# Kernel tuning notes

Hardware: AMD Instinct MI355X
Metric: run time of the kernel (lower is better)

The kernel has to match this reference:

```python
import jax, jax.numpy as jnp
import numpy as np

LORA_SCALING = 1.0 / 4.0  # lora_alpha / lora_rank
NUM_HEADS = 16
HEAD_DIM = 64
ROPE_BASE = 20000.0


def rotate_half(x):
    x1, x2 = jnp.split(x, 2, axis=-1)
    return jnp.concatenate([-x2, x1], axis=-1)


def setup_inputs() -> dict:
    key = jax.random.key(0)
    ks = jax.random.split(key, 8)
    B, S, D = 8, 1024, 1024
    hidden_states = jax.random.normal(ks[0], (B, S, D), jnp.float32)
    attention_mask = jnp.zeros((B, 1, 1, S), jnp.float32)
    # real rotary tables (HF style: duplicated half-dim freqs)
    inv_freq = 1.0 / (ROPE_BASE ** (jnp.arange(0, HEAD_DIM, 2, dtype=jnp.float32) / HEAD_DIM))
    t = jnp.arange(S, dtype=jnp.float32)
    freqs = jnp.outer(t, inv_freq)                      # [S, hd/2]
    emb = jnp.concatenate([freqs, freqs], axis=-1)      # [S, hd]
    cos = jnp.broadcast_to(jnp.cos(emb)[None], (B, S, HEAD_DIM))
    sin = jnp.broadcast_to(jnp.sin(emb)[None], (B, S, HEAD_DIM))
    adapter_mask = jax.random.randint(ks[1], (B,), 0, 5, jnp.int32)
    Wqkv_weight = jax.random.normal(ks[2], (3 * D, D), jnp.float32) * 0.02
    Wqkv_bias = jax.random.normal(ks[3], (3 * D,), jnp.float32) * 0.02
    lora_A = jax.random.normal(ks[4], (5, 4, D), jnp.float32) * 0.02
    lora_B = jax.random.normal(ks[5], (5, 3 * D, 4), jnp.float32) * 0.02
    return dict(hidden_states=hidden_states, attention_mask=attention_mask,
                cos=cos, sin=sin, adapter_mask=adapter_mask,
                Wqkv_weight=Wqkv_weight, Wqkv_bias=Wqkv_bias,
                lora_A=lora_A, lora_B=lora_B)


def reference(hidden_states, attention_mask, cos, sin, adapter_mask,
              Wqkv_weight, Wqkv_bias, lora_A, lora_B):
    B, S, D = hidden_states.shape
    H, hd = NUM_HEADS, HEAD_DIM
    # fused QKV projection with per-task LoRA (gather adapters per batch row)
    base = jnp.einsum('bsd,od->bso', hidden_states, Wqkv_weight) + Wqkv_bias
    A_t = lora_A[adapter_mask]                    # [B, r, D]
    B_t = lora_B[adapter_mask]                    # [B, 3D, r]
    lo = jnp.einsum('bsd,brd->bsr', hidden_states, A_t)
    delta = jnp.einsum('bsr,bor->bso', lo, B_t) * LORA_SCALING
    qkv = (base + delta).reshape(B, S, 3, H, hd)
    q = qkv[:, :, 0].transpose(0, 2, 1, 3)        # [B,H,S,hd]
    k = qkv[:, :, 1].transpose(0, 2, 1, 3)
    v = qkv[:, :, 2].transpose(0, 2, 1, 3)
    # inline RoPE
    c = cos[:, None, :, :]
    s = sin[:, None, :, :]
    q = q * c + rotate_half(q) * s
    k = k * c + rotate_half(k) * s
    # eager SDPA
    scaling = hd ** -0.5
    scores = jnp.einsum('bhqd,bhkd->bhqk', q, k) * scaling + attention_mask
    attn = jax.nn.softmax(scores, axis=-1)
    out = jnp.einsum('bhqk,bhkd->bhqd', attn, v)
    return out.transpose(0, 2, 1, 3).reshape(B, S, H * hd)
```

## Files before the change

### kernel.cpp

```cpp
#include <hip/hip_runtime.h>
#include <hip/hip_bf16.h>
#include <stdint.h>

typedef __attribute__((ext_vector_type(8))) short short8;
typedef __attribute__((ext_vector_type(4))) float f32x4;
typedef unsigned short ushort_t;

#define MFMA16(a, b, c) __builtin_amdgcn_mfma_f32_16x16x32_bf16((a), (b), (c), 0, 0, 0)
#define EXP2F(x) __builtin_amdgcn_exp2f(x)


__device__ __forceinline__ float bf2f(unsigned short u) {
    union { unsigned int i; float f; } x; x.i = ((unsigned int)u) << 16; return x.f;
}
__device__ __forceinline__ unsigned short f2bf(float f) {
    union { float f; unsigned int i; } x; x.f = f;
    unsigned int i = x.i;
    i = i + 0x7FFFu + ((i >> 16) & 1u);
    return (unsigned short)(i >> 16);
}
__device__ __forceinline__ unsigned int pack2(float a, float b) {
    return (unsigned int)f2bf(a) | ((unsigned int)f2bf(b) << 16);
}
__device__ __forceinline__ void glds16(const void* gsrc, void* ldst) {
    __builtin_amdgcn_global_load_lds(
        (const __attribute__((address_space(1))) unsigned int*)gsrc,
        (__attribute__((address_space(3))) unsigned int*)ldst, 16, 0, 0);
}

__global__ __launch_bounds__(64) void prep_kernel(
    const float* __restrict__ hidden,
    const float* __restrict__ W,
    const float* __restrict__ loraA,
    const int* __restrict__ adapter_mask,
    ushort_t* __restrict__ Hb,
    ushort_t* __restrict__ Wb,
    float4* __restrict__ lo)
{
    int blk = blockIdx.x;
    int lane = threadIdx.x;
    if (blk < 8192) {
        int b = blk >> 10;
        int a = adapter_mask[b];
        const float* hp = hidden + (size_t)blk * 1024 + lane * 16;
        float hv[16];
        for (int j = 0; j < 16; ++j) hv[j] = hp[j];
        uint4 p0, p1;
        p0.x = pack2(hv[0], hv[1]);  p0.y = pack2(hv[2], hv[3]);
        p0.z = pack2(hv[4], hv[5]);  p0.w = pack2(hv[6], hv[7]);
        p1.x = pack2(hv[8], hv[9]);  p1.y = pack2(hv[10], hv[11]);
        p1.z = pack2(hv[12], hv[13]); p1.w = pack2(hv[14], hv[15]);
        uint4* hd = (uint4*)(Hb + (size_t)blk * 1024 + lane * 16);
        hd[0] = p0; hd[1] = p1;
        const float* Ap = loraA + (size_t)a * 4096 + lane * 16;
        float acc[4];
        for (int r = 0; r < 4; ++r) {
            const float* ap = Ap + r * 1024;
            float s = 0.f;
            for (int j = 0; j < 16; ++j) s += hv[j] * ap[j];
            acc[r] = s;
        }
        for (int off = 32; off > 0; off >>= 1)
            for (int r = 0; r < 4; ++r) acc[r] += __shfl_xor(acc[r], off);
        if (lane == 0) lo[blk] = make_float4(acc[0], acc[1], acc[2], acc[3]);
    } else {
        int row = blk - 8192;
        const float* wp = W + (size_t)row * 1024 + lane * 16;
        float wv[16];
        for (int j = 0; j < 16; ++j) wv[j] = wp[j];
        uint4 p0, p1;
        p0.x = pack2(wv[0], wv[1]);  p0.y = pack2(wv[2], wv[3]);
        p0.z = pack2(wv[4], wv[5]);  p0.w = pack2(wv[6], wv[7]);
        p1.x = pack2(wv[8], wv[9]);  p1.y = pack2(wv[10], wv[11]);
        p1.z = pack2(wv[12], wv[13]); p1.w = pack2(wv[14], wv[15]);
        uint4* wd = (uint4*)(Wb + (size_t)row * 1024 + lane * 16);
        wd[0] = p0; wd[1] = p1;
    }
}

__global__ __launch_bounds__(256) void qkv_gemm_kernel(
    const ushort_t* __restrict__ Hb,
    const ushort_t* __restrict__ Wb,
    const float* __restrict__ bias,
    const float4* __restrict__ lo,
    const float* __restrict__ loraB,
    const int* __restrict__ adapter_mask,
    const float* __restrict__ cosp,
    const float* __restrict__ sinp,
    ushort_t* __restrict__ qw,
    ushort_t* __restrict__ kw,
    ushort_t* __restrict__ vt)
{
    __shared__ __align__(16) ushort_t As[128 * 32];
    __shared__ __align__(16) ushort_t Bs[128 * 32];
    int tid = threadIdx.x;
    int wave = tid >> 6, lane = tid & 63, quad = lane >> 4, l16 = lane & 15;
    int n0 = blockIdx.x * 128;
    int m0 = blockIdx.y * 128;
    int mq = (wave >> 1) * 64, nq = (wave & 1) * 64;

    f32x4 acc[4][4];
    for (int i = 0; i < 4; ++i) for (int j = 0; j < 4; ++j) acc[i][j] = (f32x4)0.f;

    const ushort_t* gA0 = Hb + (size_t)(m0 + (tid >> 2)) * 1024 + (tid & 3) * 8;
    const ushort_t* gA1 = gA0 + (size_t)64 * 1024;
    const ushort_t* gB0 = Wb + (size_t)(n0 + (tid >> 2)) * 1024 + (tid & 3) * 8;
    const ushort_t* gB1 = gB0 + (size_t)64 * 1024;
    char* ldsA0 = (char*)As + wave * 1024;
    char* ldsA1 = ldsA0 + 4096;
    char* ldsB0 = (char*)Bs + wave * 1024;
    char* ldsB1 = ldsB0 + 4096;

    for (int kk = 0; kk < 1024; kk += 32) {
        glds16(gA0 + kk, ldsA0);
        glds16(gA1 + kk, ldsA1);
        glds16(gB0 + kk, ldsB0);
        glds16(gB1 + kk, ldsB1);
        __syncthreads();
        short8 af[4], bf[4];
        for (int mi = 0; mi < 4; ++mi)
            af[mi] = *(const short8*)&As[(mq + mi * 16 + l16) * 32 + quad * 8];
        for (int ni = 0; ni < 4; ++ni)
            bf[ni] = *(const short8*)&Bs[(nq + ni * 16 + l16) * 32 + quad * 8];
        for (int mi = 0; mi < 4; ++mi)
            for (int ni = 0; ni < 4; ++ni)
                acc[mi][ni] = MFMA16(af[mi], bf[ni], acc[mi][ni]);
        __syncthreads();
    }

    int t = n0 >> 10;
    int b = m0 >> 10;
    int a = adapter_mask[b];
    float bi[4], bb[4][4];
    int cpos[4], chh[4];
    for (int ni = 0; ni < 4; ++ni) {
        int c = n0 + nq + ni * 16 + l16;
        bi[ni] = bias[c];
        const float* Bp = loraB + ((size_t)a * 3072 + c) * 4;
        bb[ni][0] = Bp[0]; bb[ni][1] = Bp[1]; bb[ni][2] = Bp[2]; bb[ni][3] = Bp[3];
        cpos[ni] = c & 63; chh[ni] = (c >> 6) & 15;
    }
    for (int mi = 0; mi < 4; ++mi) {
        float vals[4][4];
        for (int r = 0; r < 4; ++r) {
            int m = m0 + mq + mi * 16 + quad * 4 + r;
            float4 lov = lo[m];
            for (int ni = 0; ni < 4; ++ni)
                vals[r][ni] = acc[mi][ni][r] + bi[ni]
                      + 0.25f * (lov.x * bb[ni][0] + lov.y * bb[ni][1]
                               + lov.z * bb[ni][2] + lov.w * bb[ni][3]);
        }
        int s0 = (m0 + mq + mi * 16 + quad * 4) & 1023;
        if (t < 2) {
            for (int r = 0; r < 4; ++r) {
                int s = s0 + r;
                size_t cb = ((size_t)b * 1024 + s) * 64;
                float cA = cosp[cb + l16],      sA = sinp[cb + l16];
                float cB = cosp[cb + 16 + l16], sB = sinp[cb + 16 + l16];
                float w0 = vals[r][0] * cA - vals[r][2] * sA;
                float w2 = vals[r][2] * cA + vals[r][0] * sA;
                float w1 = vals[r][1] * cB - vals[r][3] * sB;
                float w3 = vals[r][3] * cB + vals[r][1] * sB;
                float v[4] = {w0, w1, w2, w3};
                for (int ni = 0; ni < 4; ++ni) {
                    size_t bh = (size_t)b * 16 + chh[ni];
                    ushort_t ob = f2bf(v[ni]);
                    if (t == 0) qw[(bh * 1024 + s) * 64 + cpos[ni]] = ob;
                    else        kw[(bh * 1024 + s) * 64 + cpos[ni]] = ob;
                }
            }
        } else {
            for (int ni = 0; ni < 4; ++ni) {
                uint2 pk;
                pk.x = pack2(vals[0][ni], vals[1][ni]);
                pk.y = pack2(vals[2][ni], vals[3][ni]);
                size_t bh = (size_t)b * 16 + chh[ni];
                *(uint2*)&vt[(bh * 64 + cpos[ni]) * 1024 + s0] = pk;
            }
        }
    }
}

__global__ __launch_bounds__(256) void attn_kernel(
    const ushort_t* __restrict__ qw,
    const ushort_t* __restrict__ kw,
    const ushort_t* __restrict__ vt,
    const float* __restrict__ mask,
    float* __restrict__ out)
{
    __shared__ __align__(16) ushort_t Kt[2][4096];
    __shared__ __align__(16) ushort_t Vt[2][4096];
    __shared__ __align__(16) ushort_t Ps[4][32][72];
    __shared__ float mlds[1024];
    const float KSCALE = 0.125f * 1.44269504f;
    int tid = threadIdx.x;
    int wave = tid >> 6, lane = tid & 63, quad = lane >> 4, l16 = lane & 15;
    int id = blockIdx.x;
    int qt = id >> 7;
    int bh = id & 127;
    int b = bh >> 4, h = bh & 15;
    size_t base = (size_t)bh * 65536;
    int q0 = qt * 128 + wave * 32;

    for (int i = tid; i < 1024; i += 256) mlds[i] = mask[b * 1024 + i] * 1.44269504f;

    const ushort_t* kbase = kw + base;
    const ushort_t* vbase = vt + base;

    int n0 = tid, n1 = tid + 256;
    int r0 = n0 >> 3, c0 = (n0 & 7) ^ (r0 & 7);
    int r1 = n1 >> 3, c1 = (n1 & 7) ^ (r1 & 7);
    char* kd0[2] = { (char*)&Kt[0][0] + wave * 1024, (char*)&Kt[1][0] + wave * 1024 };
    char* vd0[2] = { (char*)&Vt[0][0] + wave * 1024, (char*)&Vt[1][0] + wave * 1024 };

    short8 qf[2][2];
    for (int mt = 0; mt < 2; ++mt)
        for (int kt = 0; kt < 2; ++kt)
            qf[mt][kt] = *(const short8*)(qw + base + (size_t)(q0 + mt * 16 + l16) * 64 + kt * 32 + quad * 8);

    f32x4 oacc[2][4], sum_acc[2];
    for (int mt = 0; mt < 2; ++mt) {
        sum_acc[mt] = (f32x4)0.f;
        for (int nt = 0; nt < 4; ++nt) oacc[mt][nt] = (f32x4)0.f;
    }

    short8 ones;
    for (int j = 0; j < 8; ++j) ones[j] = (short)0x3F80;

    glds16(kbase + (size_t)r0 * 64 + c0 * 8, kd0[0]);
    glds16(kbase + (size_t)r1 * 64 + c1 * 8, kd0[0] + 4096);
    glds16(vbase + (size_t)r0 * 1024 + c0 * 8, vd0[0]);
    glds16(vbase + (size_t)r1 * 1024 + c1 * 8, vd0[0] + 4096);

    int koff[4][2], voff[4][2];
    for (int nt = 0; nt < 4; ++nt)
        for (int kt = 0; kt < 2; ++kt) {
            int rr = nt * 16 + l16;
            int cc = (kt * 4 + quad) ^ (rr & 7);
            koff[nt][kt] = (rr * 8 + cc) * 8;
            voff[nt][kt] = (rr * 8 + cc) * 8;
        }

    for (int it = 0; it < 16; ++it) {
        int cur = it & 1;
        int kt0 = it * 64;
        __syncthreads();
        if (it < 15) {
            int kn = kt0 + 64;
            int nxt = cur ^ 1;
            glds16(kbase + (size_t)(kn + r0) * 64 + c0 * 8, kd0[nxt]);
            glds16(kbase + (size_t)(kn + r1) * 64 + c1 * 8, kd0[nxt] + 4096);
            glds16(vbase + (size_t)r0 * 1024 + kn + c0 * 8, vd0[nxt]);
            glds16(vbase + (size_t)r1 * 1024 + kn + c1 * 8, vd0[nxt] + 4096);
        }
        short8 kf[4][2];
        for (int nt = 0; nt < 4; ++nt)
            for (int kt = 0; kt < 2; ++kt)
                kf[nt][kt] = *(const short8*)&Kt[cur][koff[nt][kt]];
        f32x4 sacc[2][4];
        for (int mt = 0; mt < 2; ++mt)
            for (int nt = 0; nt < 4; ++nt) {
                f32x4 z = (f32x4)0.f;
                z = MFMA16(qf[mt][0], kf[nt][0], z);
                z = MFMA16(qf[mt][1], kf[nt][1], z);
                sacc[mt][nt] = z;
            }
        float mv[4];
        for (int nt = 0; nt < 4; ++nt) mv[nt] = mlds[kt0 + nt * 16 + l16];
        for (int mt = 0; mt < 2; ++mt)
            for (int nt = 0; nt < 4; ++nt)
                for (int r = 0; r < 4; ++r) {
                    float p = EXP2F(sacc[mt][nt][r] * KSCALE + mv[nt]);
                    Ps[wave][mt * 16 + quad * 4 + r][nt * 16 + l16] = f2bf(p);
                }
        short8 pf[2][2];
        for (int mt = 0; mt < 2; ++mt)
            for (int kt = 0; kt < 2; ++kt)
                pf[mt][kt] = *(const short8*)&Ps[wave][mt * 16 + l16][kt * 32 + quad * 8];
        short8 vf[4][2];
        for (int nt = 0; nt < 4; ++nt)
            for (int kt = 0; kt < 2; ++kt)
                vf[nt][kt] = *(const short8*)&Vt[cur][voff[nt][kt]];
        for (int mt = 0; mt < 2; ++mt) {
            for (int nt = 0; nt < 4; ++nt) {
                oacc[mt][nt] = MFMA16(pf[mt][0], vf[nt][0], oacc[mt][nt]);
                oacc[mt][nt] = MFMA16(pf[mt][1], vf[nt][1], oacc[mt][nt]);
            }
            sum_acc[mt] = MFMA16(pf[mt][0], ones, sum_acc[mt]);
            sum_acc[mt] = MFMA16(pf[mt][1], ones, sum_acc[mt]);
        }
    }

    for (int mt = 0; mt < 2; ++mt) {
        for (int r = 0; r < 4; ++r) {
            float inv = 1.f / sum_acc[mt][r];
            int s = q0 + mt * 16 + quad * 4 + r;
            size_t ob = ((size_t)b * 1024 + s) * 1024 + h * 64;
            for (int nt = 0; nt < 4; ++nt)
                out[ob + nt * 16 + l16] = oacc[mt][nt][r] * inv;
        }
    }
}

extern "C" void kernel_launch(void* const* d_in, const int* in_sizes, int n_in,
                              void* d_out, int out_size, void* d_ws, size_t ws_size,
                              hipStream_t stream)
{
    const float* hidden = (const float*)d_in[0];
    const float* mask   = (const float*)d_in[1];
    const float* cosp   = (const float*)d_in[2];
    const float* sinp   = (const float*)d_in[3];
    const int* adapter_mask = (const int*)d_in[4];
    const float* W      = (const float*)d_in[5];
    const float* bias   = (const float*)d_in[6];
    const float* loraA  = (const float*)d_in[7];
    const float* loraB  = (const float*)d_in[8];
    float* out = (float*)d_out;

    char* ws = (char*)d_ws;
    float4* lo = (float4*)ws;
    ushort_t* qw = (ushort_t*)(ws + (1 << 20));
    ushort_t* kw = qw + (size_t)8 * 16 * 1024 * 64;
    ushort_t* vt = kw + (size_t)8 * 16 * 1024 * 64;

    ushort_t* Hb = (ushort_t*)d_out;
    ushort_t* Wb = Hb + (size_t)8192 * 1024;

    prep_kernel<<<11264, 64, 0, stream>>>(hidden, W, loraA, adapter_mask, Hb, Wb, lo);
    qkv_gemm_kernel<<<dim3(24, 64), 256, 0, stream>>>(Hb, Wb, bias, lo, loraB, adapter_mask,
                                                      cosp, sinp, qw, kw, vt);
    attn_kernel<<<1024, 256, 0, stream>>>(qw, kw, vt, mask, out);
}
```

Before: 259.8 us.

## Restructure QKV GEMM with double-buffered LDS, larger tiles, swizzle and XCD remap

Rewrites the QKV projection GEMM to use 256x128 block tiles with 512 threads and a K-step of 64. Global-to-LDS loads are double-buffered and split across two half-steps, so the next tile's loads overlap the MFMAs on the current one. It also adds an XOR swizzle on the LDS layout to avoid bank conflicts, raises MFMA wave priority, and remaps block IDs so neighbouring tiles are grouped across the 8 XCDs. The cost is more LDS use (96 KB per block) and hand-written waitcnt and barrier sequencing.

```diff
diff --git a/kernel.cpp b/kernel.cpp
--- a/kernel.cpp
+++ b/kernel.cpp
@@ -8,6 +8,7 @@
 
 #define MFMA16(a, b, c) __builtin_amdgcn_mfma_f32_16x16x32_bf16((a), (b), (c), 0, 0, 0)
 #define EXP2F(x) __builtin_amdgcn_exp2f(x)
+#define BARRIER() asm volatile("s_barrier" ::: "memory")
 
 
 __device__ __forceinline__ float bf2f(unsigned short u) {
@@ -78,7 +79,7 @@
     }
 }
 
-__global__ __launch_bounds__(256) void qkv_gemm_kernel(
+__global__ __launch_bounds__(512, 2) void qkv_gemm_kernel(
     const ushort_t* __restrict__ Hb,
     const ushort_t* __restrict__ Wb,
     const float* __restrict__ bias,
@@ -91,85 +92,161 @@
     ushort_t* __restrict__ kw,
     ushort_t* __restrict__ vt)
 {
-    __shared__ __align__(16) ushort_t As[128 * 32];
-    __shared__ __align__(16) ushort_t Bs[128 * 32];
+    __shared__ __align__(16) ushort_t As[2 * 256 * 64];
+    __shared__ __align__(16) ushort_t Bs[2 * 128 * 64];
     int tid = threadIdx.x;
     int wave = tid >> 6, lane = tid & 63, quad = lane >> 4, l16 = lane & 15;
-    int n0 = blockIdx.x * 128;
-    int m0 = blockIdx.y * 128;
-    int mq = (wave >> 1) * 64, nq = (wave & 1) * 64;
+    int wm = wave >> 1, wn = wave & 1;
+
+    int wg = (blockIdx.x & 7) * 96 + (blockIdx.x >> 3);
+    int bx = wg % 24, by = wg / 24;
+    int n0 = bx * 128;
+    int m0 = by * 256;
+
+#define MKSRC(P, BASEPTR, ROWOFF, N) \
+    { int r_ = (N) >> 3; int c_ = ((N) & 7) ^ (r_ & 7); \
+      P = (BASEPTR) + (size_t)((ROWOFF) + r_) * 1024 + c_ * 8; }
+    const ushort_t *pA0, *pA1, *pA2, *pA3, *pB0, *pB1;
+    MKSRC(pA0, Hb, m0, tid);
+    MKSRC(pA1, Hb, m0, tid + 512);
+    MKSRC(pA2, Hb, m0, tid + 1024);
+    MKSRC(pA3, Hb, m0, tid + 1536);
+    MKSRC(pB0, Wb, n0, tid);
+    MKSRC(pB1, Wb, n0, tid + 512);
+#undef MKSRC
+
+    char* dA = (char*)As + wave * 1024;
+    char* dB = (char*)Bs + wave * 1024;
+
+    int offA[4][2], offB[4][2];
+#pragma unroll
+    for (int mi = 0; mi < 4; ++mi)
+#pragma unroll
+        for (int kh = 0; kh < 2; ++kh) {
+            int r = wm * 64 + mi * 16 + l16;
+            int c = (kh * 4 + quad) ^ (r & 7);
+            offA[mi][kh] = (r * 8 + c) * 16;
+            r = wn * 64 + mi * 16 + l16;
+            c = (kh * 4 + quad) ^ (r & 7);
+            offB[mi][kh] = (r * 8 + c) * 16;
+        }
 
     f32x4 acc[4][4];
-    for (int i = 0; i < 4; ++i) for (int j = 0; j < 4; ++j) acc[i][j] = (f32x4)0.f;
-
-    const ushort_t* gA0 = Hb + (size_t)(m0 + (tid >> 2)) * 1024 + (tid & 3) * 8;
-    const ushort_t* gA1 = gA0 + (size_t)64 * 1024;
-    const ushort_t* gB0 = Wb + (size_t)(n0 + (tid >> 2)) * 1024 + (tid & 3) * 8;
-    const ushort_t* gB1 = gB0 + (size_t)64 * 1024;
-    char* ldsA0 = (char*)As + wave * 1024;
-    char* ldsA1 = ldsA0 + 4096;
-    char* ldsB0 = (char*)Bs + wave * 1024;
-    char* ldsB1 = ldsB0 + 4096;
-
-    for (int kk = 0; kk < 1024; kk += 32) {
-        glds16(gA0 + kk, ldsA0);
-        glds16(gA1 + kk, ldsA1);
-        glds16(gB0 + kk, ldsB0);
-        glds16(gB1 + kk, ldsB1);
-        __syncthreads();
-        short8 af[4], bf[4];
+#pragma unroll
+    for (int i = 0; i < 4; ++i)
+#pragma unroll
+        for (int j = 0; j < 4; ++j) acc[i][j] = (f32x4)0.f;
+
+    glds16(pA0, dA);
+    glds16(pA1, dA + 8192);
+    glds16(pA2, dA + 16384);
+    glds16(pA3, dA + 24576);
+    glds16(pB0, dB);
+    glds16(pB1, dB + 8192);
+
+    const char* rbA = (const char*)As;
+    const char* rbB = (const char*)Bs;
+
+    for (int t = 0; t < 16; ++t) {
+        int cur = t & 1;
+        int kn = (t + 1) * 64;
+        char* sA = dA + (cur ^ 1) * 32768;
+        char* sB = dB + (cur ^ 1) * 16384;
+        if (t < 15) {
+            glds16(pA0 + kn, sA);
+            glds16(pA1 + kn, sA + 8192);
+            glds16(pB0 + kn, sB);
+            asm volatile("s_waitcnt vmcnt(3)" ::: "memory");
+        } else {
+            asm volatile("s_waitcnt vmcnt(0)" ::: "memory");
+        }
+        BARRIER();
+        const char* bufA = rbA + cur * 32768;
+        const char* bufB = rbB + cur * 16384;
+        short8 af[4][2], bf[4][2];
+#pragma unroll
+        for (int mi = 0; mi < 4; ++mi) {
+            af[mi][0] = *(const short8*)(bufA + offA[mi][0]);
+            af[mi][1] = *(const short8*)(bufA + offA[mi][1]);
+        }
+#pragma unroll
+        for (int ni = 0; ni < 4; ++ni) {
+            bf[ni][0] = *(const short8*)(bufB + offB[ni][0]);
+            bf[ni][1] = *(const short8*)(bufB + offB[ni][1]);
+        }
+        __builtin_amdgcn_s_setprio(1);
+#pragma unroll
         for (int mi = 0; mi < 4; ++mi)
-            af[mi] = *(const short8*)&As[(mq + mi * 16 + l16) * 32 + quad * 8];
-        for (int ni = 0; ni < 4; ++ni)
-            bf[ni] = *(const short8*)&Bs[(nq + ni * 16 + l16) * 32 + quad * 8];
+#pragma unroll
+            for (int ni = 0; ni < 4; ++ni)
+                acc[mi][ni] = MFMA16(af[mi][0], bf[ni][0], acc[mi][ni]);
+        __builtin_amdgcn_s_setprio(0);
+        BARRIER();
+        if (t < 15) {
+            glds16(pA2 + kn, sA + 16384);
+            glds16(pA3 + kn, sA + 24576);
+            glds16(pB1 + kn, sB + 8192);
+        }
+        BARRIER();
+        __builtin_amdgcn_s_setprio(1);
+#pragma unroll
         for (int mi = 0; mi < 4; ++mi)
+#pragma unroll
             for (int ni = 0; ni < 4; ++ni)
-                acc[mi][ni] = MFMA16(af[mi], bf[ni], acc[mi][ni]);
-        __syncthreads();
-    }
-
-    int t = n0 >> 10;
+                acc[mi][ni] = MFMA16(af[mi][1], bf[ni][1], acc[mi][ni]);
+        __builtin_amdgcn_s_setprio(0);
+        BARRIER();
+    }
+
+    int t_qkv = n0 >> 10;
     int b = m0 >> 10;
-    int a = adapter_mask[b];
+    int a_idx = adapter_mask[b];
     float bi[4], bb[4][4];
     int cpos[4], chh[4];
+#pragma unroll
     for (int ni = 0; ni < 4; ++ni) {
-        int c = n0 + nq + ni * 16 + l16;
+        int c = n0 + wn * 64 + ni * 16 + l16;
         bi[ni] = bias[c];
-        const float* Bp = loraB + ((size_t)a * 3072 + c) * 4;
+        const float* Bp = loraB + ((size_t)a_idx * 3072 + c) * 4;
         bb[ni][0] = Bp[0]; bb[ni][1] = Bp[1]; bb[ni][2] = Bp[2]; bb[ni][3] = Bp[3];
         cpos[ni] = c & 63; chh[ni] = (c >> 6) & 15;
     }
+#pragma unroll
     for (int mi = 0; mi < 4; ++mi) {
         float vals[4][4];
+        int mrow0 = m0 + wm * 64 + mi * 16 + quad * 4;
+#pragma unroll
         for (int r = 0; r < 4; ++r) {
-            int m = m0 + mq + mi * 16 + quad * 4 + r;
-            float4 lov = lo[m];
+            float4 lov = lo[mrow0 + r];
+#pragma unroll
             for (int ni = 0; ni < 4; ++ni)
                 vals[r][ni] = acc[mi][ni][r] + bi[ni]
                       + 0.25f * (lov.x * bb[ni][0] + lov.y * bb[ni][1]
                                + lov.z * bb[ni][2] + lov.w * bb[ni][3]);
         }
-        int s0 = (m0 + mq + mi * 16 + quad * 4) & 1023;
-        if (t < 2) {
+        int s0 = mrow0 & 1023;
+        if (t_qkv < 2) {
+#pragma unroll
             for (int r = 0; r < 4; ++r) {
                 int s = s0 + r;
                 size_t cb = ((size_t)b * 1024 + s) * 64;
-                float cA = cosp[cb + l16],      sA = sinp[cb + l16];
-                float cB = cosp[cb + 16 + l16], sB = sinp[cb + 16 + l16];
-                float w0 = vals[r][0] * cA - vals[r][2] * sA;
-                float w2 = vals[r][2] * cA + vals[r][0] * sA;
-                float w1 = vals[r][1] * cB - vals[r][3] * sB;
-                float w3 = vals[r][3] * cB + vals[r][1] * sB;
+                float cA = cosp[cb + l16],      sA_ = sinp[cb + l16];
+                float cB = cosp[cb + 16 + l16], sB_ = sinp[cb + 16 + l16];
+                float w0 = vals[r][0] * cA - vals[r][2] * sA_;
+                float w2 = vals[r][2] * cA + vals[r][0] * sA_;
+                float w1 = vals[r][1] * cB - vals[r][3] * sB_;
+                float w3 = vals[r][3] * cB + vals[r][1] * sB_;
                 float v[4] = {w0, w1, w2, w3};
+#pragma unroll
                 for (int ni = 0; ni < 4; ++ni) {
                     size_t bh = (size_t)b * 16 + chh[ni];
                     ushort_t ob = f2bf(v[ni]);
-                    if (t == 0) qw[(bh * 1024 + s) * 64 + cpos[ni]] = ob;
-                    else        kw[(bh * 1024 + s) * 64 + cpos[ni]] = ob;
+                    if (t_qkv == 0) qw[(bh * 1024 + s) * 64 + cpos[ni]] = ob;
+                    else            kw[(bh * 1024 + s) * 64 + cpos[ni]] = ob;
                 }
             }
         } else {
+#pragma unroll
             for (int ni = 0; ni < 4; ++ni) {
                 uint2 pk;
                 pk.x = pack2(vals[0][ni], vals[1][ni]);
@@ -327,7 +404,7 @@
     ushort_t* Wb = Hb + (size_t)8192 * 1024;
 
     prep_kernel<<<11264, 64, 0, stream>>>(hidden, W, loraA, adapter_mask, Hb, Wb, lo);
-    qkv_gemm_kernel<<<dim3(24, 64), 256, 0, stream>>>(Hb, Wb, bias, lo, loraB, adapter_mask,
-                                                      cosp, sinp, qw, kw, vt);
+    qkv_gemm_kernel<<<768, 512, 0, stream>>>(Hb, Wb, bias, lo, loraB, adapter_mask,
+                                             cosp, sinp, qw, kw, vt);
     attn_kernel<<<1024, 256, 0, stream>>>(qw, kw, vt, mask, out);
 }
```

New measurement: 253.8 us. -2.3%, faster.

## Rewrite QKV GEMM with 256x256 tiles, double-buffered swizzled LDS, and staged prefetch

Applied to the files above, without the earlier changes.

The QKV projection GEMM moves from 128x128 tiles, 256 threads and K-step 32 with two barriers per step to 256x256 tiles, 512 threads and K-step 64. LDS is now double-buffered with an XOR swizzle, and the next tile's A and B loads are issued in phases between MFMA groups, tracked with explicit vmcnt/lgkmcnt waits and setprio. Blocks are remapped in an XCD-aware order for L2 locality. The aim is to raise arithmetic intensity and hide global load latency. The cost is heavy register pressure (128 accumulator floats per lane) and 128KB of LDS per block, which may limit occupancy.

```diff
diff --git a/kernel.cpp b/kernel.cpp
--- a/kernel.cpp
+++ b/kernel.cpp
@@ -8,6 +8,9 @@
 
 #define MFMA16(a, b, c) __builtin_amdgcn_mfma_f32_16x16x32_bf16((a), (b), (c), 0, 0, 0)
 #define EXP2F(x) __builtin_amdgcn_exp2f(x)
+#define BAR() __builtin_amdgcn_s_barrier()
+#define LGKM0() do { asm volatile("s_waitcnt lgkmcnt(0)" ::: "memory"); \
+                     __builtin_amdgcn_sched_barrier(0); } while (0)
 
 
 __device__ __forceinline__ float bf2f(unsigned short u) {
@@ -78,7 +81,7 @@
     }
 }
 
-__global__ __launch_bounds__(256) void qkv_gemm_kernel(
+__global__ __launch_bounds__(512, 2) void qkv_gemm_kernel(
     const ushort_t* __restrict__ Hb,
     const ushort_t* __restrict__ Wb,
     const float* __restrict__ bias,
@@ -91,85 +94,176 @@
     ushort_t* __restrict__ kw,
     ushort_t* __restrict__ vt)
 {
-    __shared__ __align__(16) ushort_t As[128 * 32];
-    __shared__ __align__(16) ushort_t Bs[128 * 32];
+    __shared__ __align__(16) ushort_t As[2][16384];
+    __shared__ __align__(16) ushort_t Bs[2][16384];
     int tid = threadIdx.x;
     int wave = tid >> 6, lane = tid & 63, quad = lane >> 4, l16 = lane & 15;
-    int n0 = blockIdx.x * 128;
-    int m0 = blockIdx.y * 128;
-    int mq = (wave >> 1) * 64, nq = (wave & 1) * 64;
-
-    f32x4 acc[4][4];
-    for (int i = 0; i < 4; ++i) for (int j = 0; j < 4; ++j) acc[i][j] = (f32x4)0.f;
-
-    const ushort_t* gA0 = Hb + (size_t)(m0 + (tid >> 2)) * 1024 + (tid & 3) * 8;
-    const ushort_t* gA1 = gA0 + (size_t)64 * 1024;
-    const ushort_t* gB0 = Wb + (size_t)(n0 + (tid >> 2)) * 1024 + (tid & 3) * 8;
-    const ushort_t* gB1 = gB0 + (size_t)64 * 1024;
-    char* ldsA0 = (char*)As + wave * 1024;
-    char* ldsA1 = ldsA0 + 4096;
-    char* ldsB0 = (char*)Bs + wave * 1024;
-    char* ldsB1 = ldsB0 + 4096;
-
-    for (int kk = 0; kk < 1024; kk += 32) {
-        glds16(gA0 + kk, ldsA0);
-        glds16(gA1 + kk, ldsA1);
-        glds16(gB0 + kk, ldsB0);
-        glds16(gB1 + kk, ldsB1);
-        __syncthreads();
-        short8 af[4], bf[4];
-        for (int mi = 0; mi < 4; ++mi)
-            af[mi] = *(const short8*)&As[(mq + mi * 16 + l16) * 32 + quad * 8];
-        for (int ni = 0; ni < 4; ++ni)
-            bf[ni] = *(const short8*)&Bs[(nq + ni * 16 + l16) * 32 + quad * 8];
-        for (int mi = 0; mi < 4; ++mi)
-            for (int ni = 0; ni < 4; ++ni)
-                acc[mi][ni] = MFMA16(af[mi], bf[ni], acc[mi][ni]);
-        __syncthreads();
-    }
-
-    int t = n0 >> 10;
+    int wm = wave >> 2, wn = wave & 3;
+
+    int wg = (blockIdx.x & 7) * 48 + (blockIdx.x >> 3);
+    int bx = wg % 12, by = wg / 12;
+    int n0 = bx * 256;
+    int m0 = by * 256;
+
+    int r_ = tid >> 3, c_ = (tid & 7) ^ (r_ & 7);
+    const ushort_t* pA0 = Hb + (size_t)(m0 +   0 + r_) * 1024 + c_ * 8;
+    const ushort_t* pA1 = Hb + (size_t)(m0 +  64 + r_) * 1024 + c_ * 8;
+    const ushort_t* pA2 = Hb + (size_t)(m0 + 128 + r_) * 1024 + c_ * 8;
+    const ushort_t* pA3 = Hb + (size_t)(m0 + 192 + r_) * 1024 + c_ * 8;
+    const ushort_t* pB0 = Wb + (size_t)(n0 +   0 + r_) * 1024 + c_ * 8;
+    const ushort_t* pB1 = Wb + (size_t)(n0 +  64 + r_) * 1024 + c_ * 8;
+    const ushort_t* pB2 = Wb + (size_t)(n0 + 128 + r_) * 1024 + c_ * 8;
+    const ushort_t* pB3 = Wb + (size_t)(n0 + 192 + r_) * 1024 + c_ * 8;
+    char* stA0 = (char*)&As[0][0] + wave * 1024;
+    char* stB0 = (char*)&Bs[0][0] + wave * 1024;
+
+    f32x4 acc[8][4];
+#pragma unroll
+    for (int i = 0; i < 8; ++i)
+#pragma unroll
+        for (int j = 0; j < 4; ++j) acc[i][j] = (f32x4)0.f;
+
+    glds16(pB0, stB0);          glds16(pB1, stB0 + 8192);
+    glds16(pB2, stB0 + 16384);  glds16(pB3, stB0 + 24576);
+    glds16(pA0, stA0);          glds16(pA1, stA0 + 8192);
+    glds16(pA2, stA0 + 16384);  glds16(pA3, stA0 + 24576);
+    glds16(pB0 + 64, stB0 + 32768);          glds16(pB1 + 64, stB0 + 32768 + 8192);
+    glds16(pB2 + 64, stB0 + 32768 + 16384);  glds16(pB3 + 64, stB0 + 32768 + 24576);
+
+    short8 bfr[4][2];
+    short8 af0[2], af1[2];
+
+#define AREADS(p) do {                                                              \
+        int rl0 = (p) * 32 + l16;                                                   \
+        int rl1 = rl0 + 16;                                                         \
+        int u0 = wm * 2 + (rl0 >> 6), u1 = wm * 2 + (rl1 >> 6);                     \
+        int rr0 = rl0 & 63, rr1 = rl1 & 63;                                         \
+        af0[0] = *(const short8*)(rdA + u0 * 8192 + (rr0 * 8 + ((quad    ) ^ (rr0 & 7))) * 16); \
+        af0[1] = *(const short8*)(rdA + u0 * 8192 + (rr0 * 8 + ((quad + 4) ^ (rr0 & 7))) * 16); \
+        af1[0] = *(const short8*)(rdA + u1 * 8192 + (rr1 * 8 + ((quad    ) ^ (rr1 & 7))) * 16); \
+        af1[1] = *(const short8*)(rdA + u1 * 8192 + (rr1 * 8 + ((quad + 4) ^ (rr1 & 7))) * 16); \
+    } while (0)
+
+#define PMFMA(p) do {                                                    \
+        __builtin_amdgcn_s_setprio(1);                                   \
+        acc[2*(p)  ][0] = MFMA16(af0[0], bfr[0][0], acc[2*(p)  ][0]);    \
+        acc[2*(p)  ][1] = MFMA16(af0[0], bfr[1][0], acc[2*(p)  ][1]);    \
+        acc[2*(p)  ][2] = MFMA16(af0[0], bfr[2][0], acc[2*(p)  ][2]);    \
+        acc[2*(p)  ][3] = MFMA16(af0[0], bfr[3][0], acc[2*(p)  ][3]);    \
+        acc[2*(p)+1][0] = MFMA16(af1[0], bfr[0][0], acc[2*(p)+1][0]);    \
+        acc[2*(p)+1][1] = MFMA16(af1[0], bfr[1][0], acc[2*(p)+1][1]);    \
+        acc[2*(p)+1][2] = MFMA16(af1[0], bfr[2][0], acc[2*(p)+1][2]);    \
+        acc[2*(p)+1][3] = MFMA16(af1[0], bfr[3][0], acc[2*(p)+1][3]);    \
+        acc[2*(p)  ][0] = MFMA16(af0[1], bfr[0][1], acc[2*(p)  ][0]);    \
+        acc[2*(p)  ][1] = MFMA16(af0[1], bfr[1][1], acc[2*(p)  ][1]);    \
+        acc[2*(p)  ][2] = MFMA16(af0[1], bfr[2][1], acc[2*(p)  ][2]);    \
+        acc[2*(p)  ][3] = MFMA16(af0[1], bfr[3][1], acc[2*(p)  ][3]);    \
+        acc[2*(p)+1][0] = MFMA16(af1[1], bfr[0][1], acc[2*(p)+1][0]);    \
+        acc[2*(p)+1][1] = MFMA16(af1[1], bfr[1][1], acc[2*(p)+1][1]);    \
+        acc[2*(p)+1][2] = MFMA16(af1[1], bfr[2][1], acc[2*(p)+1][2]);    \
+        acc[2*(p)+1][3] = MFMA16(af1[1], bfr[3][1], acc[2*(p)+1][3]);    \
+        __builtin_amdgcn_s_setprio(0);                                   \
+    } while (0)
+
+#pragma unroll 2
+    for (int t = 0; t < 16; ++t) {
+        int cur = t & 1;
+        const char* rdA = (const char*)&As[0][0] + cur * 32768;
+        const char* rdB = (const char*)&Bs[0][0] + cur * 32768;
+        char* sA = stA0 + (cur ^ 1) * 32768;
+        char* sB = stB0 + cur * 32768;
+        int kA = (t + 1) << 6;
+        int kB = (t + 2) << 6;
+        bool doA = (t < 15), doB = (t < 14);
+
+        if (t < 15) { asm volatile("s_waitcnt vmcnt(4)" ::: "memory"); }
+        else        { asm volatile("s_waitcnt vmcnt(0)" ::: "memory"); }
+        BAR();
+#pragma unroll
+        for (int ni = 0; ni < 4; ++ni) {
+            int rb = ni * 16 + l16;
+            bfr[ni][0] = *(const short8*)(rdB + wn * 8192 + (rb * 8 + ((quad    ) ^ (rb & 7))) * 16);
+            bfr[ni][1] = *(const short8*)(rdB + wn * 8192 + (rb * 8 + ((quad + 4) ^ (rb & 7))) * 16);
+        }
+        AREADS(0);
+        if (doA) { glds16(pA0 + kA, sA); glds16(pA1 + kA, sA + 8192); }
+        BAR();
+        LGKM0();
+        PMFMA(0);
+
+        BAR();
+        AREADS(1);
+        if (doA) { glds16(pA2 + kA, sA + 16384); glds16(pA3 + kA, sA + 24576); }
+        BAR();
+        LGKM0();
+        PMFMA(1);
+
+        BAR();
+        AREADS(2);
+        if (doB) { glds16(pB0 + kB, sB); glds16(pB1 + kB, sB + 8192); }
+        BAR();
+        LGKM0();
+        PMFMA(2);
+
+        BAR();
+        AREADS(3);
+        if (doB) { glds16(pB2 + kB, sB + 16384); glds16(pB3 + kB, sB + 24576); }
+        BAR();
+        LGKM0();
+        PMFMA(3);
+    }
+#undef AREADS
+#undef PMFMA
+
+    int t_qkv = n0 >> 10;
     int b = m0 >> 10;
-    int a = adapter_mask[b];
+    int a_idx = adapter_mask[b];
     float bi[4], bb[4][4];
     int cpos[4], chh[4];
+#pragma unroll
     for (int ni = 0; ni < 4; ++ni) {
-        int c = n0 + nq + ni * 16 + l16;
+        int c = n0 + wn * 64 + ni * 16 + l16;
         bi[ni] = bias[c];
-        const float* Bp = loraB + ((size_t)a * 3072 + c) * 4;
+        const float* Bp = loraB + ((size_t)a_idx * 3072 + c) * 4;
         bb[ni][0] = Bp[0]; bb[ni][1] = Bp[1]; bb[ni][2] = Bp[2]; bb[ni][3] = Bp[3];
         cpos[ni] = c & 63; chh[ni] = (c >> 6) & 15;
     }
-    for (int mi = 0; mi < 4; ++mi) {
+#pragma unroll
+    for (int mi = 0; mi < 8; ++mi) {
         float vals[4][4];
+        int mrow0 = m0 + wm * 128 + mi * 16 + quad * 4;
+#pragma unroll
         for (int r = 0; r < 4; ++r) {
-            int m = m0 + mq + mi * 16 + quad * 4 + r;
-            float4 lov = lo[m];
+            float4 lov = lo[mrow0 + r];
+#pragma unroll
             for (int ni = 0; ni < 4; ++ni)
                 vals[r][ni] = acc[mi][ni][r] + bi[ni]
                       + 0.25f * (lov.x * bb[ni][0] + lov.y * bb[ni][1]
                                + lov.z * bb[ni][2] + lov.w * bb[ni][3]);
         }
-        int s0 = (m0 + mq + mi * 16 + quad * 4) & 1023;
-        if (t < 2) {
+        int s0 = mrow0 & 1023;
+        if (t_qkv < 2) {
+#pragma unroll
             for (int r = 0; r < 4; ++r) {
                 int s = s0 + r;
                 size_t cb = ((size_t)b * 1024 + s) * 64;
-                float cA = cosp[cb + l16],      sA = sinp[cb + l16];
-                float cB = cosp[cb + 16 + l16], sB = sinp[cb + 16 + l16];
-                float w0 = vals[r][0] * cA - vals[r][2] * sA;
-                float w2 = vals[r][2] * cA + vals[r][0] * sA;
-                float w1 = vals[r][1] * cB - vals[r][3] * sB;
-                float w3 = vals[r][3] * cB + vals[r][1] * sB;
+                float cA = cosp[cb + l16],      sA_ = sinp[cb + l16];
+                float cB = cosp[cb + 16 + l16], sB_ = sinp[cb + 16 + l16];
+                float w0 = vals[r][0] * cA - vals[r][2] * sA_;
+                float w2 = vals[r][2] * cA + vals[r][0] * sA_;
+                float w1 = vals[r][1] * cB - vals[r][3] * sB_;
+                float w3 = vals[r][3] * cB + vals[r][1] * sB_;
                 float v[4] = {w0, w1, w2, w3};
+#pragma unroll
                 for (int ni = 0; ni < 4; ++ni) {
                     size_t bh = (size_t)b * 16 + chh[ni];
                     ushort_t ob = f2bf(v[ni]);
-                    if (t == 0) qw[(bh * 1024 + s) * 64 + cpos[ni]] = ob;
-                    else        kw[(bh * 1024 + s) * 64 + cpos[ni]] = ob;
+                    if (t_qkv == 0) qw[(bh * 1024 + s) * 64 + cpos[ni]] = ob;
+                    else            kw[(bh * 1024 + s) * 64 + cpos[ni]] = ob;
                 }
             }
         } else {
+#pragma unroll
             for (int ni = 0; ni < 4; ++ni) {
                 uint2 pk;
                 pk.x = pack2(vals[0][ni], vals[1][ni]);
@@ -327,7 +421,7 @@
     ushort_t* Wb = Hb + (size_t)8192 * 1024;
 
     prep_kernel<<<11264, 64, 0, stream>>>(hidden, W, loraA, adapter_mask, Hb, Wb, lo);
-    qkv_gemm_kernel<<<dim3(24, 64), 256, 0, stream>>>(Hb, Wb, bias, lo, loraB, adapter_mask,
-                                                      cosp, sinp, qw, kw, vt);
+    qkv_gemm_kernel<<<384, 512, 0, stream>>>(Hb, Wb, bias, lo, loraB, adapter_mask,
+                                             cosp, sinp, qw, kw, vt);
     attn_kernel<<<1024, 256, 0, stream>>>(qw, kw, vt, mask, out);
 }
```

After: 253.8 us. 2.3% less time.
